# Performance work log

Measured on AMD Instinct MI355X. Metric: run time of the kernel, lower is better.

## Reference

```python
import jax, jax.numpy as jnp
import numpy as np

SOFTCAP = 50.0  # GEMMA2_TANH_SCALE
N_HEADS = 16

def _rope(x, cos, sin):
    # x: [B,S,H,D]; cos/sin: [S,D/2]; interleaved complex pairs as in apply_rotary_emb
    x0 = x[..., 0::2]
    x1 = x[..., 1::2]
    c = cos[None, :, None, :]
    s = sin[None, :, None, :]
    r0 = x0 * c - x1 * s
    r1 = x0 * s + x1 * c
    return jnp.stack([r0, r1], axis=-1).reshape(x.shape)

def setup_inputs() -> dict:
    key = jax.random.key(0)
    ks = jax.random.split(key, 5)
    B, S, DM = 1, 2048, 2048
    hd = DM // N_HEADS
    scale = 1.0 / np.sqrt(DM)
    x = jax.random.normal(ks[0], (B, S, DM), jnp.float32)
    wq = jax.random.normal(ks[1], (DM, DM), jnp.float32) * scale
    wk = jax.random.normal(ks[2], (DM, DM), jnp.float32) * scale
    wv = jax.random.normal(ks[3], (DM, DM), jnp.float32) * scale
    wo = jax.random.normal(ks[4], (DM, DM), jnp.float32) * scale
    # rotary tables, theta=10000 as in llama
    inv_freq = 10000.0 ** (-jnp.arange(0, hd, 2, dtype=jnp.float32) / hd)
    ang = jnp.arange(S, dtype=jnp.float32)[:, None] * inv_freq[None, :]
    return {"x": x, "wq": wq, "wk": wk, "wv": wv, "wo": wo,
            "freqs_cos": jnp.cos(ang), "freqs_sin": jnp.sin(ang)}

def reference(x, wq, wk, wv, wo, freqs_cos, freqs_sin):
    B, S, DM = x.shape
    H = N_HEADS
    hd = DM // H
    q = (x @ wq).reshape(B, S, H, hd)
    k = (x @ wk).reshape(B, S, H, hd)
    v = (x @ wv).reshape(B, S, H, hd)
    q = _rope(q, freqs_cos, freqs_sin)
    k = _rope(k, freqs_cos, freqs_sin)
    # scores [B,H,S,S]
    scores = jnp.einsum('bqhd,bkhd->bhqk', q, k) / jnp.sqrt(jnp.float32(hd))
    scores = SOFTCAP * jnp.tanh(scores / SOFTCAP)  # gemma2 tanh soft-cap
    causal = jnp.tril(jnp.ones((S, S), dtype=bool))
    scores = jnp.where(causal[None, None], scores, -jnp.inf)
    p = jax.nn.softmax(scores, axis=-1)
    o = jnp.einsum('bhqk,bkhd->bqhd', p, v).reshape(B, S, DM)
    return o @ wo
```

## Files before the change

### kernel.cpp

```cpp
#include <hip/hip_runtime.h>
#include <hip/hip_bf16.h>

typedef __attribute__((ext_vector_type(8))) short short8;
typedef __attribute__((ext_vector_type(4))) short short4v;
typedef __attribute__((ext_vector_type(4))) float f32x4;
typedef __attribute__((ext_vector_type(4))) float float4v;

#define S_LEN 2048
#define DMODEL 2048
#define N_HEADS 16
#define HEAD_DIM 128
#define NKT 32

__device__ __forceinline__ float bf2f(__hip_bfloat16 b) { return __bfloat162float(b); }
__device__ __forceinline__ __hip_bfloat16 f2bf(float f) { return __float2bfloat16(f); }
__device__ __forceinline__ short bfs(float f) {
    union { __hip_bfloat16 b; short s; } x; x.b = __float2bfloat16(f); return x.s;
}
__device__ __forceinline__ float sbf(short s) {
    union { short s; __hip_bfloat16 b; } x; x.s = s; return __bfloat162float(x.b);
}

#if __has_builtin(__builtin_amdgcn_global_load_lds)
#define HAVE_ASYNC_LDS 1
#else
#define HAVE_ASYNC_LDS 0
#endif

__device__ __forceinline__ void stage16(const __hip_bfloat16* g, __hip_bfloat16* ldsbase, int lane) {
#if HAVE_ASYNC_LDS
    __builtin_amdgcn_global_load_lds(
        (const __attribute__((address_space(1))) unsigned int*)g,
        (__attribute__((address_space(3))) unsigned int*)ldsbase,
        16, 0, 0);
#else
    *(short8*)((char*)ldsbase + lane * 16) = *(const short8*)g;
#endif
}

__global__ __launch_bounds__(256) void prep(const float* __restrict__ x,
                                            const float* __restrict__ w0,
                                            const float* __restrict__ w1,
                                            const float* __restrict__ w2,
                                            const float* __restrict__ w3,
                                            __hip_bfloat16* __restrict__ xb,
                                            __hip_bfloat16* __restrict__ o0,
                                            __hip_bfloat16* __restrict__ o1,
                                            __hip_bfloat16* __restrict__ o2,
                                            __hip_bfloat16* __restrict__ o3) {
    const int z = blockIdx.z;
    const int tid = threadIdx.x;
    if (z == 4) {
        size_t base = (((size_t)blockIdx.y * 32 + blockIdx.x) * 256 + tid) * 16;
        for (int i = 0; i < 4; ++i) {
            float4v v = *(const float4v*)(x + base + i * 4);
            short4v p;
            p.x = bfs(v.x); p.y = bfs(v.y); p.z = bfs(v.z); p.w = bfs(v.w);
            *(short4v*)((short*)xb + base + i * 4) = p;
        }
        return;
    }
    const float* in = (z == 0) ? w0 : (z == 1) ? w1 : (z == 2) ? w2 : w3;
    __hip_bfloat16* out = (z == 0) ? o0 : (z == 1) ? o1 : (z == 2) ? o2 : o3;
    const int bx = blockIdx.x * 64;
    const int by = blockIdx.y * 64;
    const int sr = tid >> 4;
    const int sc = tid & 15;
    float4v v[4];
#pragma unroll
    for (int i = 0; i < 4; ++i)
        v[i] = *(const float4v*)(in + (size_t)(by + 4 * sr + i) * DMODEL + bx + 4 * sc);
#pragma unroll
    for (int j = 0; j < 4; ++j) {
        short4v p;
        p.x = bfs(v[0][j]);
        p.y = bfs(v[1][j]);
        p.z = bfs(v[2][j]);
        p.w = bfs(v[3][j]);
        *(short4v*)((short*)out + (size_t)(bx + 4 * sc + j) * DMODEL + by + 4 * sr) = p;
    }
}


#define CFENCE asm volatile("" ::: "memory")
#define BARRIER do { CFENCE; __builtin_amdgcn_s_barrier(); CFENCE; } while (0)
#define WAIT_LGKM0 asm volatile("s_waitcnt lgkmcnt(0)" ::: "memory")
#define WAIT_VM(n) asm volatile("s_waitcnt vmcnt(" #n ")" ::: "memory")

#define STAGE_A8(buf, half, kt) do {                                                        \
    const __hip_bfloat16* gpA_ = A + (size_t)(m0 + (half) * 128 + wave * 16 + rsel) * DMODEL \
                                 + (kt) * 64 + gsrc;                                        \
    __hip_bfloat16* lpA_ = (__hip_bfloat16*)(smem + ((buf) * 2 + (half)) * 8192 + wave * 1024); \
    stage16(gpA_, lpA_, lane);                                                              \
    stage16(gpA_ + (size_t)8 * DMODEL, lpA_ + 512, lane);                                   \
} while (0)

#define STAGE_B8(buf, half, kt) do {                                                        \
    const __hip_bfloat16* gpB_ = Bt + (size_t)(n0 + (half) * 128 + wave * 16 + rsel) * DMODEL \
                                 + (kt) * 64 + gsrc;                                        \
    __hip_bfloat16* lpB_ = (__hip_bfloat16*)(smem + 32768 + ((buf) * 2 + (half)) * 8192 + wave * 1024); \
    stage16(gpB_, lpB_, lane);                                                              \
    stage16(gpB_ + (size_t)8 * DMODEL, lpB_ + 512, lane);                                   \
} while (0)

#define LDA_ALL(buf) do {                                                                   \
    const char* ab_ = (const char*)(smem + ((buf) * 2 + wr) * 8192);                        \
    _Pragma("unroll")                                                                       \
    for (int mt_ = 0; mt_ < 8; ++mt_) {                                                     \
        const int rowL_ = mt_ * 16 + lane15;                                                \
        const int r7_ = rowL_ & 7;                                                          \
        af[mt_][0] = *(const short8*)(ab_ + rowL_ * 128 + ((quad ^ r7_) * 16));             \
        af[mt_][1] = *(const short8*)(ab_ + rowL_ * 128 + (((4 + quad) ^ r7_) * 16));       \
    }                                                                                       \
} while (0)

#define LDB_ALL(buf) do {                                                                   \
    const char* bb_ = (const char*)(smem + 32768 + ((buf) * 2 + hb) * 8192);                \
    _Pragma("unroll")                                                                       \
    for (int nt_ = 0; nt_ < 4; ++nt_) {                                                     \
        const int rowL_ = wc1 * 64 + nt_ * 16 + lane15;                                     \
        const int r7_ = rowL_ & 7;                                                          \
        bfr[nt_][0] = *(const short8*)(bb_ + rowL_ * 128 + ((quad ^ r7_) * 16));            \
        bfr[nt_][1] = *(const short8*)(bb_ + rowL_ * 128 + (((4 + quad) ^ r7_) * 16));      \
    }                                                                                       \
} while (0)

#define MFMAQ(mb, nb) do {                                                                  \
    _Pragma("unroll")                                                                       \
    for (int mt_ = 0; mt_ < 4; ++mt_) {                                                     \
        _Pragma("unroll")                                                                   \
        for (int nt_ = 0; nt_ < 2; ++nt_) {                                                 \
            acc[(mb) + mt_][(nb) + nt_] = __builtin_amdgcn_mfma_f32_16x16x32_bf16(          \
                af[(mb) + mt_][0], bfr[(nb) + nt_][0], acc[(mb) + mt_][(nb) + nt_], 0, 0, 0); \
            acc[(mb) + mt_][(nb) + nt_] = __builtin_amdgcn_mfma_f32_16x16x32_bf16(          \
                af[(mb) + mt_][1], bfr[(nb) + nt_][1], acc[(mb) + mt_][(nb) + nt_], 0, 0, 0); \
        }                                                                                   \
    }                                                                                       \
} while (0)

#define GROUP(g, cur, nxt) do {                                                             \
    const int g_ = (g);                                                                     \
    const bool stB_ = (g_ + 1 < NKT);                                                       \
    const bool stA_ = (g_ + 2 < NKT);                                                       \
    LDA_ALL(cur);                                                                           \
    LDB_ALL(cur);                                                                           \
    if (stB_) { STAGE_B8(nxt, 0, g_ + 1); STAGE_B8(nxt, 1, g_ + 1); }                       \
    __builtin_amdgcn_s_setprio(1);                                                          \
    MFMAQ(0, 0); MFMAQ(4, 0);                                                               \
    __builtin_amdgcn_s_setprio(0);                                                          \
    WAIT_LGKM0;                                                                             \
    BARRIER;                                                                                \
    if (stA_) { STAGE_A8(cur, 0, g_ + 2); STAGE_A8(cur, 1, g_ + 2); }                       \
    __builtin_amdgcn_s_setprio(1);                                                          \
    MFMAQ(0, 2); MFMAQ(4, 2);                                                               \
    __builtin_amdgcn_s_setprio(0);                                                          \
    if (stA_) { WAIT_VM(4); }                                                               \
    else if (stB_) { WAIT_VM(0); }                                                          \
    BARRIER;                                                                                \
} while (0)

__global__ __launch_bounds__(512, 2) void gemm_qkv_8ph(const __hip_bfloat16* __restrict__ A,
                                                       const __hip_bfloat16* __restrict__ Bq,
                                                       const __hip_bfloat16* __restrict__ Bk,
                                                       const __hip_bfloat16* __restrict__ Bv,
                                                       __hip_bfloat16* __restrict__ Cq,
                                                       __hip_bfloat16* __restrict__ Ck,
                                                       __hip_bfloat16* __restrict__ Cvt,
                                                       const float* __restrict__ fc,
                                                       const float* __restrict__ fs) {
    __shared__ alignas(16) short smem[65536];

    const int tid = threadIdx.x;
    const int wave = tid >> 6;
    const int lane = tid & 63;
    const int lane15 = lane & 15;
    const int quad = lane >> 4;
    const int wr = wave >> 2;
    const int wc = wave & 3;
    const int wc1 = wc & 1;
    const int hb = wc >> 1;
    const int rsel = lane >> 3;
    const int gsrc = ((lane & 7) ^ rsel) * 8;

    const int which = blockIdx.x >> 3;
    const int n0 = (blockIdx.x & 7) * 256;
    const int m0 = blockIdx.y * 256;
    const __hip_bfloat16* Bt = (which == 0) ? Bq : (which == 1) ? Bk : Bv;

    short8 af[8][2];
    short8 bfr[4][2];
    f32x4 acc[8][4];

    STAGE_A8(0, 0, 0);
    STAGE_B8(0, 0, 0);
    STAGE_A8(0, 1, 0);
    STAGE_B8(0, 1, 0);
    STAGE_A8(1, 0, 1);
    STAGE_A8(1, 1, 1);
#pragma unroll
    for (int i = 0; i < 8; ++i)
#pragma unroll
        for (int j = 0; j < 4; ++j)
            acc[i][j] = {0.f, 0.f, 0.f, 0.f};
    WAIT_VM(4);
    BARRIER;

#pragma unroll 1
    for (int g = 0; g < NKT; g += 2) {
        GROUP(g, 0, 1);
        GROUP(g + 1, 1, 0);
    }

    if (which < 2) {
        __hip_bfloat16* C = (which == 0) ? Cq : Ck;
#pragma unroll
        for (int mt = 0; mt < 8; ++mt)
#pragma unroll
            for (int nt = 0; nt < 4; ++nt) {
                int col = n0 + wc * 64 + nt * 16 + lane15;
                int j = (col & 127) >> 1;
                bool odd = col & 1;
#pragma unroll
                for (int i = 0; i < 4; ++i) {
                    int row = m0 + wr * 128 + mt * 16 + quad * 4 + i;
                    float v = acc[mt][nt][i];
                    float p = __shfl_xor(v, 1, 64);
                    float c = fc[row * 64 + j];
                    float sn = fs[row * 64 + j];
                    float r = odd ? (p * sn + v * c) : (v * c - p * sn);
                    C[(size_t)row * DMODEL + col] = f2bf(r);
                }
            }
    } else {
#pragma unroll
        for (int mt = 0; mt < 8; ++mt) {
            int rowbase = m0 + wr * 128 + mt * 16 + quad * 4;
#pragma unroll
            for (int nt = 0; nt < 4; ++nt) {
                int col = n0 + wc * 64 + nt * 16 + lane15;
                short4v pk;
                pk.x = bfs(acc[mt][nt][0]);
                pk.y = bfs(acc[mt][nt][1]);
                pk.z = bfs(acc[mt][nt][2]);
                pk.w = bfs(acc[mt][nt][3]);
                *(short4v*)((short*)Cvt + (size_t)col * S_LEN + rowbase) = pk;
            }
        }
    }
}

__global__ __launch_bounds__(256) void gemm_out(const __hip_bfloat16* __restrict__ A,
                                                const __hip_bfloat16* __restrict__ Bt,
                                                float* __restrict__ C) {
    __shared__ alignas(16) __hip_bfloat16 As[2][128 * 32];
    __shared__ alignas(16) __hip_bfloat16 Bs[2][64 * 32];
    const int tid = threadIdx.x;
    const int wave = tid >> 6;
    const int lane = tid & 63;
    const int lane15 = lane & 15;
    const int quad = lane >> 4;
    const int m0 = blockIdx.y * 128;
    const int n0 = blockIdx.x * 64;
    const int wm = (wave >> 1) * 64;
    const int wn = (wave & 1) * 32;
    f32x4 acc[4][2];
    for (int i = 0; i < 4; ++i)
        for (int j = 0; j < 2; ++j)
            acc[i][j] = {0.f, 0.f, 0.f, 0.f};
    const int rA = lane >> 2;
    const int cA = (lane & 3) * 8;
    for (int k0 = 0; k0 < DMODEL; k0 += 64) {
        __syncthreads();
        for (int h = 0; h < 2; ++h) {
            int kk = k0 + h * 32;
            for (int c = 0; c < 3; ++c) {
                int chunk = wave * 3 + c;
                if (chunk < 8) {
                    int r = chunk * 16 + rA;
                    stage16(A + (size_t)(m0 + r) * DMODEL + kk + cA, As[h] + chunk * 512, lane);
                } else {
                    int r = (chunk - 8) * 16 + rA;
                    stage16(Bt + (size_t)(n0 + r) * DMODEL + kk + cA, Bs[h] + (chunk - 8) * 512, lane);
                }
            }
        }
#if HAVE_ASYNC_LDS
        asm volatile("s_waitcnt vmcnt(0)" ::: "memory");
#endif
        __syncthreads();
        for (int h = 0; h < 2; ++h) {
            short8 af[4], bfr[2];
            for (int mt = 0; mt < 4; ++mt)
                af[mt] = *(const short8*)(As[h] + (wm + mt * 16 + lane15) * 32 + quad * 8);
            for (int nt = 0; nt < 2; ++nt)
                bfr[nt] = *(const short8*)(Bs[h] + (wn + nt * 16 + lane15) * 32 + quad * 8);
            for (int mt = 0; mt < 4; ++mt)
                for (int nt = 0; nt < 2; ++nt)
                    acc[mt][nt] = __builtin_amdgcn_mfma_f32_16x16x32_bf16(af[mt], bfr[nt], acc[mt][nt], 0, 0, 0);
        }
    }
    for (int mt = 0; mt < 4; ++mt)
        for (int nt = 0; nt < 2; ++nt)
            for (int i = 0; i < 4; ++i) {
                int row = m0 + wm + mt * 16 + quad * 4 + i;
                int col = n0 + wn + nt * 16 + lane15;
                C[(size_t)row * DMODEL + col] = acc[mt][nt][i];
            }
}

__global__ __launch_bounds__(256) void flash_attn(const __hip_bfloat16* __restrict__ Q,
                                                  const __hip_bfloat16* __restrict__ Kb,
                                                  const __hip_bfloat16* __restrict__ Vt,
                                                  float* __restrict__ N0,
                                                  float* __restrict__ N1,
                                                  float* __restrict__ L0,
                                                  float* __restrict__ L1) {
    __shared__ alignas(16) short Ks[32][136];
    __shared__ alignas(16) short Vs[128][40];
    __shared__ alignas(16) short Pl[4][16][40];
    const int tid = threadIdx.x;
    const int wave = tid >> 6;
    const int lane = tid & 63;
    const int lane15 = lane & 15;
    const int quad = lane >> 4;
    const int bx = blockIdx.x;
    const int chunk = bx >> 9;
    const int bxl = bx & 511;
    const int u = bxl & 255;
    const int head = u & 15;
    const int qp = u >> 4;
    const int qb = (bxl < 256) ? (31 - qp) : qp;
    const int q0w = qb * 64 + wave * 16;
    const int k_lo = chunk ? (qb + 1) : 0;
    const int k_hi = chunk ? (2 * qb + 2) : (qb + 1);
    const float K1 = 0.08838834764831845f * (1.0f / 25.0f);

    float* __restrict__ Nw = chunk ? N1 : N0;
    float* __restrict__ Lw = chunk ? L1 : L0;

    const __hip_bfloat16* Qh = Q + (size_t)q0w * DMODEL + head * HEAD_DIM;
    short8 qf[4];
    for (int kk = 0; kk < 4; ++kk)
        qf[kk] = *(const short8*)(Qh + (size_t)lane15 * DMODEL + kk * 32 + quad * 8);

    f32x4 acc[8];
    for (int i = 0; i < 8; ++i) acc[i] = {0.f, 0.f, 0.f, 0.f};
    float lpart[4] = {0.f, 0.f, 0.f, 0.f};

    const int krow = tid >> 3, kcol = (tid & 7) * 16;
    const int vrow = tid >> 1, vcol = (tid & 1) * 16;
    const __hip_bfloat16* Kg = Kb + (size_t)krow * DMODEL + head * HEAD_DIM + kcol;
    const __hip_bfloat16* Vg = Vt + (size_t)(head * HEAD_DIM + vrow) * S_LEN + vcol;

    const int kb0 = k_lo * 32;
    short8 gk0 = *(const short8*)(Kg + (size_t)kb0 * DMODEL);
    short8 gk1 = *(const short8*)(Kg + (size_t)kb0 * DMODEL + 8);
    short8 gv0 = *(const short8*)(Vg + kb0);
    short8 gv1 = *(const short8*)(Vg + kb0 + 8);

    for (int kt = k_lo; kt < k_hi; ++kt) {
        const int kb = kt * 32;
        __syncthreads();
        *(short8*)&Ks[krow][kcol] = gk0;
        *(short8*)&Ks[krow][kcol + 8] = gk1;
        *(short8*)&Vs[vrow][vcol] = gv0;
        *(short8*)&Vs[vrow][vcol + 8] = gv1;
        __syncthreads();

        if (kt + 1 < k_hi) {
            const __hip_bfloat16* Kg2 = Kg + (size_t)(kb + 32) * DMODEL;
            const __hip_bfloat16* Vg2 = Vg + kb + 32;
            gk0 = *(const short8*)(Kg2);
            gk1 = *(const short8*)(Kg2 + 8);
            gv0 = *(const short8*)(Vg2);
            gv1 = *(const short8*)(Vg2 + 8);
        }

        if (kb <= q0w + 15) {
            f32x4 sc[2];
            sc[0] = {0.f, 0.f, 0.f, 0.f};
            sc[1] = {0.f, 0.f, 0.f, 0.f};
            for (int c = 0; c < 2; ++c)
                for (int kk = 0; kk < 4; ++kk) {
                    short8 kf = *(const short8*)&Ks[c * 16 + lane15][kk * 32 + quad * 8];
                    sc[c] = __builtin_amdgcn_mfma_f32_16x16x32_bf16(qf[kk], kf, sc[c], 0, 0, 0);
                }

            const bool masked = (kb + 31 > q0w);
            const int key0 = kb + lane15;
            const int key1 = kb + 16 + lane15;
            for (int i = 0; i < 4; ++i) {
                float e0 = __expf(sc[0][i] * K1);
                float e1 = __expf(sc[1][i] * K1);
                float c0 = __builtin_fmaf(-100.0f, __builtin_amdgcn_rcpf(e0 + 1.0f), 40.0f);
                float c1 = __builtin_fmaf(-100.0f, __builtin_amdgcn_rcpf(e1 + 1.0f), 40.0f);
                float p0 = __expf(c0);
                float p1 = __expf(c1);
                if (masked) {
                    int q = q0w + quad * 4 + i;
                    if (key0 > q) p0 = 0.f;
                    if (key1 > q) p1 = 0.f;
                }
                short b0 = bfs(p0), b1 = bfs(p1);
                lpart[i] += sbf(b0) + sbf(b1);
                Pl[wave][quad * 4 + i][lane15] = b0;
                Pl[wave][quad * 4 + i][16 + lane15] = b1;
            }
            asm volatile("s_waitcnt lgkmcnt(0)" ::: "memory");
            short8 pf = *(const short8*)&Pl[wave][lane15][quad * 8];
            asm volatile("" ::: "memory");
            for (int nt = 0; nt < 8; ++nt) {
                short8 vf = *(const short8*)&Vs[nt * 16 + lane15][quad * 8];
                acc[nt] = __builtin_amdgcn_mfma_f32_16x16x32_bf16(pf, vf, acc[nt], 0, 0, 0);
            }
        }
    }

    for (int i = 0; i < 4; ++i) {
        float l = lpart[i];
        l += __shfl_xor(l, 1, 64);
        l += __shfl_xor(l, 2, 64);
        l += __shfl_xor(l, 4, 64);
        l += __shfl_xor(l, 8, 64);
        int row = q0w + quad * 4 + i;
        if (lane15 == 0) Lw[(head << 11) + row] = l;
        for (int nt = 0; nt < 8; ++nt) {
            int col = head * HEAD_DIM + nt * 16 + lane15;
            Nw[(size_t)row * DMODEL + col] = acc[nt][i];
        }
    }
}

__global__ __launch_bounds__(256) void attn_combine(const float* __restrict__ N0,
                                                    const float* __restrict__ N1,
                                                    const float* __restrict__ L0,
                                                    const float* __restrict__ L1,
                                                    __hip_bfloat16* __restrict__ Aout) {
    size_t i0 = ((size_t)blockIdx.x * 256 + threadIdx.x) * 8;
    const int row = (int)(i0 >> 11);
    const int head = (int)((i0 >> 7) & 15);
    const float l = L0[(head << 11) + row] + L1[(head << 11) + row];
    const float inv = 1.0f / l;
    float4v a0 = *(const float4v*)(N0 + i0);
    float4v a1 = *(const float4v*)(N1 + i0);
    float4v b0 = *(const float4v*)(N0 + i0 + 4);
    float4v b1 = *(const float4v*)(N1 + i0 + 4);
    short8 o;
    ((short*)&o)[0] = bfs((a0.x + a1.x) * inv);
    ((short*)&o)[1] = bfs((a0.y + a1.y) * inv);
    ((short*)&o)[2] = bfs((a0.z + a1.z) * inv);
    ((short*)&o)[3] = bfs((a0.w + a1.w) * inv);
    ((short*)&o)[4] = bfs((b0.x + b1.x) * inv);
    ((short*)&o)[5] = bfs((b0.y + b1.y) * inv);
    ((short*)&o)[6] = bfs((b0.z + b1.z) * inv);
    ((short*)&o)[7] = bfs((b0.w + b1.w) * inv);
    *(short8*)((short*)Aout + i0) = o;
}

extern "C" void kernel_launch(void* const* d_in, const int* in_sizes, int n_in,
                              void* d_out, int out_size, void* d_ws, size_t ws_size,
                              hipStream_t stream) {
    const float* x  = (const float*)d_in[0];
    const float* wq = (const float*)d_in[1];
    const float* wk = (const float*)d_in[2];
    const float* wv = (const float*)d_in[3];
    const float* wo = (const float*)d_in[4];
    const float* fc = (const float*)d_in[5];
    const float* fs = (const float*)d_in[6];
    float* out = (float*)d_out;

    char* ws = (char*)d_ws;
    const size_t MB8 = (size_t)2048 * 2048 * sizeof(__hip_bfloat16);
    __hip_bfloat16* wq_t = (__hip_bfloat16*)(ws + 0 * MB8);
    __hip_bfloat16* wk_t = (__hip_bfloat16*)(ws + 1 * MB8);
    __hip_bfloat16* wv_t = (__hip_bfloat16*)(ws + 2 * MB8);
    __hip_bfloat16* wo_t = (__hip_bfloat16*)(ws + 3 * MB8);
    __hip_bfloat16* s4   = (__hip_bfloat16*)(ws + 4 * MB8);
    __hip_bfloat16* s5   = (__hip_bfloat16*)(ws + 5 * MB8);
    __hip_bfloat16* s6   = (__hip_bfloat16*)(ws + 6 * MB8);
    float* N1 = (float*)(ws + 7 * MB8);
    float* L0 = (float*)(ws + 9 * MB8);
    float* L1 = L0 + 2048 * 16;
    __hip_bfloat16* x_bf = (__hip_bfloat16*)d_out;
    float* N0 = (float*)d_out;

    prep<<<dim3(32, 32, 5), 256, 0, stream>>>(x, wq, wk, wv, wo, x_bf, wq_t, wk_t, wv_t, wo_t);

    gemm_qkv_8ph<<<dim3(24, 8), 512, 0, stream>>>(x_bf, wq_t, wk_t, wv_t, s4, s5, s6, fc, fs);

    flash_attn<<<1024, 256, 0, stream>>>(s4, s5, s6, N0, N1, L0, L1);

    attn_combine<<<2048, 256, 0, stream>>>(N0, N1, L0, L1, s4);
    gemm_out<<<dim3(32, 16), 256, 0, stream>>>(s4, wo_t, out);
}
```

Before: 278.3 us.

## Fuse split-K attention combine into flash kernel via atomic flags; coalesce weight transpose

Result: slower. 470.3 us (+69.0%).

```diff
diff --git a/kernel.cpp b/kernel.cpp
--- a/kernel.cpp
+++ b/kernel.cpp
@@ -47,10 +47,15 @@
                                             __hip_bfloat16* __restrict__ o0,
                                             __hip_bfloat16* __restrict__ o1,
                                             __hip_bfloat16* __restrict__ o2,
-                                            __hip_bfloat16* __restrict__ o3) {
+                                            __hip_bfloat16* __restrict__ o3,
+                                            int* __restrict__ flags) {
     const int z = blockIdx.z;
     const int tid = threadIdx.x;
     if (z == 4) {
+        if (blockIdx.x == 0 && blockIdx.y == 0) {
+            flags[tid] = 0;
+            flags[tid + 256] = 0;
+        }
         size_t base = (((size_t)blockIdx.y * 32 + blockIdx.x) * 256 + tid) * 16;
         for (int i = 0; i < 4; ++i) {
             float4v v = *(const float4v*)(x + base + i * 4);
@@ -62,6 +67,7 @@
     }
     const float* in = (z == 0) ? w0 : (z == 1) ? w1 : (z == 2) ? w2 : w3;
     __hip_bfloat16* out = (z == 0) ? o0 : (z == 1) ? o1 : (z == 2) ? o2 : o3;
+    __shared__ short T[64][68];
     const int bx = blockIdx.x * 64;
     const int by = blockIdx.y * 64;
     const int sr = tid >> 4;
@@ -77,8 +83,21 @@
         p.y = bfs(v[1][j]);
         p.z = bfs(v[2][j]);
         p.w = bfs(v[3][j]);
-        *(short4v*)((short*)out + (size_t)(bx + 4 * sc + j) * DMODEL + by + 4 * sr) = p;
-    }
+        *(short4v*)&T[4 * sc + j][4 * sr] = p;
+    }
+    __syncthreads();
+    const int orow = tid >> 2;
+    const int oc = (tid & 3) * 16;
+    short4v r0 = *(const short4v*)&T[orow][oc];
+    short4v r1 = *(const short4v*)&T[orow][oc + 4];
+    short4v r2 = *(const short4v*)&T[orow][oc + 8];
+    short4v r3 = *(const short4v*)&T[orow][oc + 12];
+    short8 a, b;
+    ((short4v*)&a)[0] = r0; ((short4v*)&a)[1] = r1;
+    ((short4v*)&b)[0] = r2; ((short4v*)&b)[1] = r3;
+    short* op = (short*)out + (size_t)(bx + orow) * DMODEL + by + oc;
+    *(short8*)op = a;
+    *(short8*)(op + 8) = b;
 }
 
 
@@ -308,16 +327,19 @@
             }
 }
 
-__global__ __launch_bounds__(256) void flash_attn(const __hip_bfloat16* __restrict__ Q,
+__global__ __launch_bounds__(256) void flash_attn(const __hip_bfloat16* Q,
                                                   const __hip_bfloat16* __restrict__ Kb,
                                                   const __hip_bfloat16* __restrict__ Vt,
                                                   float* __restrict__ N0,
                                                   float* __restrict__ N1,
                                                   float* __restrict__ L0,
-                                                  float* __restrict__ L1) {
+                                                  float* __restrict__ L1,
+                                                  int* __restrict__ flags,
+                                                  __hip_bfloat16* Aout) {
     __shared__ alignas(16) short Ks[32][136];
     __shared__ alignas(16) short Vs[128][40];
     __shared__ alignas(16) short Pl[4][16][40];
+    __shared__ int srole;
     const int tid = threadIdx.x;
     const int wave = tid >> 6;
     const int lane = tid & 63;
@@ -416,45 +438,44 @@
         }
     }
 
+    float lsum[4];
     for (int i = 0; i < 4; ++i) {
         float l = lpart[i];
         l += __shfl_xor(l, 1, 64);
         l += __shfl_xor(l, 2, 64);
         l += __shfl_xor(l, 4, 64);
         l += __shfl_xor(l, 8, 64);
+        lsum[i] = l;
+    }
+
+    for (int i = 0; i < 4; ++i) {
         int row = q0w + quad * 4 + i;
-        if (lane15 == 0) Lw[(head << 11) + row] = l;
+        if (lane15 == 0) Lw[(head << 11) + row] = lsum[i];
         for (int nt = 0; nt < 8; ++nt) {
             int col = head * HEAD_DIM + nt * 16 + lane15;
             Nw[(size_t)row * DMODEL + col] = acc[nt][i];
         }
     }
-}
-
-__global__ __launch_bounds__(256) void attn_combine(const float* __restrict__ N0,
-                                                    const float* __restrict__ N1,
-                                                    const float* __restrict__ L0,
-                                                    const float* __restrict__ L1,
-                                                    __hip_bfloat16* __restrict__ Aout) {
-    size_t i0 = ((size_t)blockIdx.x * 256 + threadIdx.x) * 8;
-    const int row = (int)(i0 >> 11);
-    const int head = (int)((i0 >> 7) & 15);
-    const float l = L0[(head << 11) + row] + L1[(head << 11) + row];
-    const float inv = 1.0f / l;
-    float4v a0 = *(const float4v*)(N0 + i0);
-    float4v a1 = *(const float4v*)(N1 + i0);
-    float4v b0 = *(const float4v*)(N0 + i0 + 4);
-    float4v b1 = *(const float4v*)(N1 + i0 + 4);
-    short8 o;
-    ((short*)&o)[0] = bfs((a0.x + a1.x) * inv);
-    ((short*)&o)[1] = bfs((a0.y + a1.y) * inv);
-    ((short*)&o)[2] = bfs((a0.z + a1.z) * inv);
-    ((short*)&o)[3] = bfs((a0.w + a1.w) * inv);
-    ((short*)&o)[4] = bfs((b0.x + b1.x) * inv);
-    ((short*)&o)[5] = bfs((b0.y + b1.y) * inv);
-    ((short*)&o)[6] = bfs((b0.z + b1.z) * inv);
-    ((short*)&o)[7] = bfs((b0.w + b1.w) * inv);
-    *(short8*)((short*)Aout + i0) = o;
+
+    __threadfence();
+    __syncthreads();
+    if (tid == 0) srole = atomicAdd(&flags[head * 32 + qb], 1) & 1;
+    __syncthreads();
+
+    if (srole) {
+        __threadfence();
+        const float* __restrict__ No = chunk ? N0 : N1;
+        const float* __restrict__ Lo = chunk ? L0 : L1;
+        for (int i = 0; i < 4; ++i) {
+            int row = q0w + quad * 4 + i;
+            float inv = 1.0f / (lsum[i] + Lo[(head << 11) + row]);
+            for (int nt = 0; nt < 8; ++nt) {
+                int col = head * HEAD_DIM + nt * 16 + lane15;
+                float o = (acc[nt][i] + No[(size_t)row * DMODEL + col]) * inv;
+                Aout[(size_t)row * DMODEL + col] = f2bf(o);
+            }
+        }
+    }
 }
 
 extern "C" void kernel_launch(void* const* d_in, const int* in_sizes, int n_in,
@@ -481,15 +502,15 @@
     float* N1 = (float*)(ws + 7 * MB8);
     float* L0 = (float*)(ws + 9 * MB8);
     float* L1 = L0 + 2048 * 16;
+    int* flags = (int*)(ws + 9 * MB8 + 256 * 1024);
     __hip_bfloat16* x_bf = (__hip_bfloat16*)d_out;
     float* N0 = (float*)d_out;
 
-    prep<<<dim3(32, 32, 5), 256, 0, stream>>>(x, wq, wk, wv, wo, x_bf, wq_t, wk_t, wv_t, wo_t);
+    prep<<<dim3(32, 32, 5), 256, 0, stream>>>(x, wq, wk, wv, wo, x_bf, wq_t, wk_t, wv_t, wo_t, flags);
 
     gemm_qkv_8ph<<<dim3(24, 8), 512, 0, stream>>>(x_bf, wq_t, wk_t, wv_t, s4, s5, s6, fc, fs);
 
-    flash_attn<<<1024, 256, 0, stream>>>(s4, s5, s6, N0, N1, L0, L1);
-
-    attn_combine<<<2048, 256, 0, stream>>>(N0, N1, L0, L1, s4);
+    flash_attn<<<1024, 256, 0, stream>>>(s4, s5, s6, N0, N1, L0, L1, flags, s4);
+
     gemm_out<<<dim3(32, 16), 256, 0, stream>>>(s4, wo_t, out);
 }
```

## Split causal attention KV range into three chunks and stage weight transpose through LDS

Applied to the files above, without the earlier changes.

New measurement: 278.6 us. Within noise of the previous version (+0.1%).

```diff
diff --git a/kernel.cpp b/kernel.cpp
--- a/kernel.cpp
+++ b/kernel.cpp
@@ -62,6 +62,7 @@
     }
     const float* in = (z == 0) ? w0 : (z == 1) ? w1 : (z == 2) ? w2 : w3;
     __hip_bfloat16* out = (z == 0) ? o0 : (z == 1) ? o1 : (z == 2) ? o2 : o3;
+    __shared__ short T[64][68];
     const int bx = blockIdx.x * 64;
     const int by = blockIdx.y * 64;
     const int sr = tid >> 4;
@@ -77,8 +78,21 @@
         p.y = bfs(v[1][j]);
         p.z = bfs(v[2][j]);
         p.w = bfs(v[3][j]);
-        *(short4v*)((short*)out + (size_t)(bx + 4 * sc + j) * DMODEL + by + 4 * sr) = p;
-    }
+        *(short4v*)&T[4 * sc + j][4 * sr] = p;
+    }
+    __syncthreads();
+    const int orow = tid >> 2;
+    const int oc = (tid & 3) * 16;
+    short4v r0 = *(const short4v*)&T[orow][oc];
+    short4v r1 = *(const short4v*)&T[orow][oc + 4];
+    short4v r2 = *(const short4v*)&T[orow][oc + 8];
+    short4v r3 = *(const short4v*)&T[orow][oc + 12];
+    short8 a, b;
+    ((short4v*)&a)[0] = r0; ((short4v*)&a)[1] = r1;
+    ((short4v*)&b)[0] = r2; ((short4v*)&b)[1] = r3;
+    short* op = (short*)out + (size_t)(bx + orow) * DMODEL + by + oc;
+    *(short8*)op = a;
+    *(short8*)(op + 8) = b;
 }
 
 
@@ -313,11 +327,13 @@
                                                   const __hip_bfloat16* __restrict__ Vt,
                                                   float* __restrict__ N0,
                                                   float* __restrict__ N1,
+                                                  float* __restrict__ N2,
                                                   float* __restrict__ L0,
-                                                  float* __restrict__ L1) {
+                                                  float* __restrict__ L1,
+                                                  float* __restrict__ L2) {
     __shared__ alignas(16) short Ks[32][136];
-    __shared__ alignas(16) short Vs[128][40];
-    __shared__ alignas(16) short Pl[4][16][40];
+    __shared__ alignas(16) short Vs[128][44];
+    __shared__ alignas(16) short Pl[4][16][44];
     const int tid = threadIdx.x;
     const int wave = tid >> 6;
     const int lane = tid & 63;
@@ -331,12 +347,14 @@
     const int qp = u >> 4;
     const int qb = (bxl < 256) ? (31 - qp) : qp;
     const int q0w = qb * 64 + wave * 16;
-    const int k_lo = chunk ? (qb + 1) : 0;
-    const int k_hi = chunk ? (2 * qb + 2) : (qb + 1);
+    const int T = 2 * qb + 2;
+    const int l0 = (T + 2) / 3, l1 = (T + 1) / 3;
+    const int k_lo = (chunk == 0) ? 0 : (chunk == 1) ? l0 : l0 + l1;
+    const int k_hi = (chunk == 0) ? l0 : (chunk == 1) ? l0 + l1 : T;
     const float K1 = 0.08838834764831845f * (1.0f / 25.0f);
 
-    float* __restrict__ Nw = chunk ? N1 : N0;
-    float* __restrict__ Lw = chunk ? L1 : L0;
+    float* __restrict__ Nw = (chunk == 0) ? N0 : (chunk == 1) ? N1 : N2;
+    float* __restrict__ Lw = (chunk == 0) ? L0 : (chunk == 1) ? L1 : L2;
 
     const __hip_bfloat16* Qh = Q + (size_t)q0w * DMODEL + head * HEAD_DIM;
     short8 qf[4];
@@ -433,27 +451,32 @@
 
 __global__ __launch_bounds__(256) void attn_combine(const float* __restrict__ N0,
                                                     const float* __restrict__ N1,
+                                                    const float* __restrict__ N2,
                                                     const float* __restrict__ L0,
                                                     const float* __restrict__ L1,
+                                                    const float* __restrict__ L2,
                                                     __hip_bfloat16* __restrict__ Aout) {
     size_t i0 = ((size_t)blockIdx.x * 256 + threadIdx.x) * 8;
     const int row = (int)(i0 >> 11);
     const int head = (int)((i0 >> 7) & 15);
-    const float l = L0[(head << 11) + row] + L1[(head << 11) + row];
+    const int li = (head << 11) + row;
+    const float l = L0[li] + L1[li] + L2[li];
     const float inv = 1.0f / l;
     float4v a0 = *(const float4v*)(N0 + i0);
     float4v a1 = *(const float4v*)(N1 + i0);
+    float4v a2 = *(const float4v*)(N2 + i0);
     float4v b0 = *(const float4v*)(N0 + i0 + 4);
     float4v b1 = *(const float4v*)(N1 + i0 + 4);
+    float4v b2 = *(const float4v*)(N2 + i0 + 4);
     short8 o;
-    ((short*)&o)[0] = bfs((a0.x + a1.x) * inv);
-    ((short*)&o)[1] = bfs((a0.y + a1.y) * inv);
-    ((short*)&o)[2] = bfs((a0.z + a1.z) * inv);
-    ((short*)&o)[3] = bfs((a0.w + a1.w) * inv);
-    ((short*)&o)[4] = bfs((b0.x + b1.x) * inv);
-    ((short*)&o)[5] = bfs((b0.y + b1.y) * inv);
-    ((short*)&o)[6] = bfs((b0.z + b1.z) * inv);
-    ((short*)&o)[7] = bfs((b0.w + b1.w) * inv);
+    ((short*)&o)[0] = bfs((a0.x + a1.x + a2.x) * inv);
+    ((short*)&o)[1] = bfs((a0.y + a1.y + a2.y) * inv);
+    ((short*)&o)[2] = bfs((a0.z + a1.z + a2.z) * inv);
+    ((short*)&o)[3] = bfs((a0.w + a1.w + a2.w) * inv);
+    ((short*)&o)[4] = bfs((b0.x + b1.x + b2.x) * inv);
+    ((short*)&o)[5] = bfs((b0.y + b1.y + b2.y) * inv);
+    ((short*)&o)[6] = bfs((b0.z + b1.z + b2.z) * inv);
+    ((short*)&o)[7] = bfs((b0.w + b1.w + b2.w) * inv);
     *(short8*)((short*)Aout + i0) = o;
 }
 
@@ -479,8 +502,10 @@
     __hip_bfloat16* s5   = (__hip_bfloat16*)(ws + 5 * MB8);
     __hip_bfloat16* s6   = (__hip_bfloat16*)(ws + 6 * MB8);
     float* N1 = (float*)(ws + 7 * MB8);
+    float* N2 = (float*)(ws + 0 * MB8);
     float* L0 = (float*)(ws + 9 * MB8);
-    float* L1 = L0 + 2048 * 16;
+    float* L1 = L0 + 32768;
+    float* L2 = L0 + 65536;
     __hip_bfloat16* x_bf = (__hip_bfloat16*)d_out;
     float* N0 = (float*)d_out;
 
@@ -488,8 +513,8 @@
 
     gemm_qkv_8ph<<<dim3(24, 8), 512, 0, stream>>>(x_bf, wq_t, wk_t, wv_t, s4, s5, s6, fc, fs);
 
-    flash_attn<<<1024, 256, 0, stream>>>(s4, s5, s6, N0, N1, L0, L1);
-
-    attn_combine<<<2048, 256, 0, stream>>>(N0, N1, L0, L1, s4);
+    flash_attn<<<1536, 256, 0, stream>>>(s4, s5, s6, N0, N1, N2, L0, L1, L2);
+
+    attn_combine<<<2048, 256, 0, stream>>>(N0, N1, N2, L0, L1, L2, s4);
     gemm_out<<<dim3(32, 16), 256, 0, stream>>>(s4, wo_t, out);
 }
```
